# Kernel optimization log

Hardware: AMD Instinct MI355X
Metric: run time of the kernel (lower is better)

## Reference

```python
import jax, jax.numpy as jnp
import numpy as np

N = 100000   # n_nodes (= ninput, identity features)
E = 1600000  # edges per adjacency (avg degree 16)
H = 128      # nhid
EPS = 1e-12


def setup_inputs() -> dict:
    key = jax.random.key(0)
    ks = jax.random.split(key, 24)
    inp = {
        'adj1_rows': jax.random.randint(ks[0], (E,), 0, N),
        'adj1_cols': jax.random.randint(ks[1], (E,), 0, N),
        'adj1_vals': jax.random.uniform(ks[2], (E,), jnp.float32) / 16.0,
        'adj2_rows': jax.random.randint(ks[3], (E,), 0, N),
        'adj2_cols': jax.random.randint(ks[4], (E,), 0, N),
        'adj2_vals': jax.random.uniform(ks[5], (E,), jnp.float32) / 16.0,
    }
    s = 1.0 / np.sqrt(H)
    inp['w1'] = jax.random.uniform(ks[6], (N, H), jnp.float32, -s, s)
    for i in range(2, 10):
        inp[f'w{i}'] = jax.random.uniform(ks[5 + i], (H, H), jnp.float32, -s, s)
    s2 = 1.0 / np.sqrt(2 * H)
    inp['m1'] = jax.random.uniform(ks[15], (H, 2 * H), jnp.float32, -s, s)
    inp['b1'] = jnp.zeros((2 * H,), jnp.float32)
    inp['m2'] = jax.random.uniform(ks[16], (2 * H, 2 * H), jnp.float32, -s2, s2)
    inp['b2'] = jnp.zeros((2 * H,), jnp.float32)
    inp['m3'] = jax.random.uniform(ks[17], (2 * H, 1), jnp.float32, -s2, s2)
    inp['b3'] = jnp.zeros((1,), jnp.float32)
    return inp


def _spmm(rows, cols, vals, x):
    # sparse [N,N] @ dense [N,H] via gather + segment_sum
    return jax.ops.segment_sum(vals[:, None] * x[cols], rows, num_segments=N)


def _l2norm(x):
    # F.normalize(x, p=2, dim=1)
    n = jnp.sqrt(jnp.sum(x * x, axis=1, keepdims=True))
    return x / jnp.maximum(n, EPS)


def _mlp(x, m1, b1, m2, b2, m3, b3):
    # dropout inactive (eval mode) for deterministic reference
    h = jax.nn.relu(x @ m1 + b1)
    h = jax.nn.relu(h @ m2 + b2)
    return h @ m3 + b3  # [N,1]


def _branch(rows, cols, vals, w1, ws, mlp_params):
    x = jax.nn.relu(_spmm(rows, cols, vals, w1))
    x = _l2norm(x)
    score = _mlp(x, *mlp_params)
    for i, w in enumerate(ws):
        x = jax.nn.relu(_spmm(rows, cols, vals, x @ w))
        if i < len(ws) - 1:  # last layer (gc9) is relu only, no normalize
            x = _l2norm(x)
        score = score + _mlp(x, *mlp_params)
    return score


def reference(adj1_rows, adj1_cols, adj1_vals, adj2_rows, adj2_cols, adj2_vals,
              w1, w2, w3, w4, w5, w6, w7, w8, w9,
              m1, b1, m2, b2, m3, b3):
    ws = [w2, w3, w4, w5, w6, w7, w8, w9]
    mlp_params = (m1, b1, m2, b2, m3, b3)
    score1 = _branch(adj1_rows, adj1_cols, adj1_vals, w1, ws, mlp_params)
    score2 = _branch(adj2_rows, adj2_cols, adj2_vals, w1, ws, mlp_params)
    return score1 * score2  # [N,1]
```

## Files before the change

kernel.cpp:

```cpp
#include <hip/hip_runtime.h>
#include <hip/hip_fp16.h>

#define NN 100000
#define NE 1600000
#define HD 128
#define HD2 256

#define NBK 512
#define RPB 196
#define CH  4096
#define CAP 4096

typedef unsigned int u32;
typedef unsigned short u16;
typedef _Float16 half8 __attribute__((ext_vector_type(8)));
typedef float floatx4 __attribute__((ext_vector_type(4)));

static inline int cdiv(int a, int b){ return (a + b - 1) / b; }

__device__ __forceinline__ u32 split_pack(float v){
  __half h;
  if(fabsf(v) < 6.103515625e-05f) h = __ushort_as_half((u16)0);
  else h = __float2half_rn(v);
  float hf = __half2float(h);
  __half l = __float2half_rn((v - hf) * 4096.0f);
  return (u32)__half_as_ushort(h) | ((u32)__half_as_ushort(l) << 16);
}

__global__ void k_setup(const float* __restrict__ w0, const float* __restrict__ w1,
                        const float* __restrict__ w2, const float* __restrict__ w3,
                        const float* __restrict__ w4, const float* __restrict__ w5,
                        const float* __restrict__ w6, const float* __restrict__ w7,
                        const float* __restrict__ m1, const float* __restrict__ m2,
                        u32* __restrict__ wbase, float* __restrict__ sc,
                        int* __restrict__ bcur){
  int bid = blockIdx.x;
  if(bid < 896){
    int idx = bid * 256 + threadIdx.x;
    const float* W; int K, N, local;
    if(idx < 131072){
      int wi = idx >> 14; local = idx & 16383; K = HD; N = HD;
      W = wi == 0 ? w0 : wi == 1 ? w1 : wi == 2 ? w2 : wi == 3 ? w3 :
          wi == 4 ? w4 : wi == 5 ? w5 : wi == 6 ? w6 : w7;
    } else if(idx < 163840){
      local = idx - 131072; K = HD; N = HD2; W = m1;
    } else {
      local = idx - 163840; K = HD2; N = HD2; W = m2;
    }
    int n = local / K, k = local - n * K;
    wbase[idx] = split_pack(W[(size_t)k * N + n]);
  } else if(bid < 896 + 782){
    int i = (bid - 896) * 256 + threadIdx.x;
    if(i < 2 * NN) sc[i] = 0.f;
  } else {
    int i = (bid - 896 - 782) * 256 + threadIdx.x;
    if(i < 2 * NBK) bcur[i] = (i & (NBK - 1)) * CAP;
  }
}

__global__ void k_binscatter(const int* __restrict__ r0a, const int* __restrict__ c0a,
                             const float* __restrict__ v0a,
                             const int* __restrict__ r1a, const int* __restrict__ c1a,
                             const float* __restrict__ v1a,
                             int* __restrict__ bcur,
                             u32* __restrict__ sr0, uint2* __restrict__ sv0,
                             u32* __restrict__ sr1, uint2* __restrict__ sv1){
  __shared__ int cnt[NBK];
  __shared__ int bstart[NBK];
  __shared__ int gbase[NBK];
  __shared__ int sh[256];
  __shared__ u32 srow[CH];
  __shared__ uint2 scvs[CH];
  int z = blockIdx.y;
  const int* rows = z ? r1a : r0a;
  const int* cols = z ? c1a : c0a;
  const float* vals = z ? v1a : v0a;
  int* cur = bcur + z * NBK;
  u32* osr = z ? sr1 : sr0;
  uint2* osv = z ? sv1 : sv0;
  int t = threadIdx.x;
  for(int i = t; i < NBK; i += 256) cnt[i] = 0;
  __syncthreads();
  int e0 = blockIdx.x * CH;
  int total = NE - e0; if(total > CH) total = CH;
  int r_[16], c_[16], b_[16], k_[16]; float v_[16];
  #pragma unroll
  for(int k = 0; k < 16; k++){
    int e = e0 + t + k * 256;
    b_[k] = -1;
    if(e < NE){
      r_[k] = rows[e]; c_[k] = cols[e]; v_[k] = vals[e];
      b_[k] = r_[k] / RPB;
      k_[k] = atomicAdd(&cnt[b_[k]], 1);
    }
  }
  __syncthreads();
  int v0 = cnt[2 * t], v1 = cnt[2 * t + 1];
  int s2 = v0 + v1;
  sh[t] = s2;
  __syncthreads();
  for(int d = 1; d < 256; d <<= 1){
    int tv = (t >= d) ? sh[t - d] : 0;
    __syncthreads();
    sh[t] += tv;
    __syncthreads();
  }
  int excl = sh[t] - s2;
  bstart[2 * t] = excl;
  bstart[2 * t + 1] = excl + v0;
  __syncthreads();
  #pragma unroll
  for(int k = 0; k < 16; k++){
    if(b_[k] >= 0){
      int slot = bstart[b_[k]] + k_[k];
      srow[slot] = (u32)r_[k];
      scvs[slot] = make_uint2((u32)c_[k], __float_as_uint(v_[k]));
    }
  }
  for(int b = t; b < NBK; b += 256){
    int c = cnt[b];
    if(c > 0) gbase[b] = atomicAdd(&cur[b], c);
  }
  __syncthreads();
  for(int i = t; i < total; i += 256){
    u32 r = srow[i];
    int b = (int)r / RPB;
    int dest = gbase[b] + (i - bstart[b]);
    osr[dest] = r;
    osv[dest] = scvs[i];
  }
}

__global__ void k_bucket_scan(const int* __restrict__ bcur, int* __restrict__ bbase,
                              int* __restrict__ c1ptr, int* __restrict__ c2ptr){
  __shared__ int sh[256];
  int z = blockIdx.x;
  const int* cur = bcur + z * NBK;
  int* bb = bbase + z * NBK;
  int t = threadIdx.x;
  int v0 = cur[2 * t]     - (2 * t) * CAP;
  int v1 = cur[2 * t + 1] - (2 * t + 1) * CAP;
  int s2 = v0 + v1;
  sh[t] = s2;
  __syncthreads();
  for(int d = 1; d < 256; d <<= 1){
    int tv = (t >= d) ? sh[t - d] : 0;
    __syncthreads();
    sh[t] += tv;
    __syncthreads();
  }
  int excl = sh[t] - s2;
  bb[2 * t] = excl;
  bb[2 * t + 1] = excl + v0;
  if(t == 0){
    int* rp = z ? c2ptr : c1ptr;
    rp[NN] = NE;
  }
}

__global__ void k_bucket_place(const int* __restrict__ bcur, const int* __restrict__ bbase,
                               const u32* __restrict__ sr0, const uint2* __restrict__ sv0,
                               const u32* __restrict__ sr1, const uint2* __restrict__ sv1,
                               int* __restrict__ c1ptr, int* __restrict__ c2ptr,
                               uint2* __restrict__ e0, uint2* __restrict__ e1){
  __shared__ int hist[RPB];
  __shared__ int cur[RPB];
  __shared__ int rs[RPB + 1];
  __shared__ int sh[256];
  __shared__ u32 srows[CAP];
  __shared__ uint2 est[CAP];
  int z = blockIdx.y;
  int b = blockIdx.x;
  int r0 = b * RPB;
  if(r0 >= NN) return;
  int rend = r0 + RPB; if(rend > NN) rend = NN;
  int nr = rend - r0;
  const u32* sr = z ? sr1 : sr0;
  const uint2* sv = z ? sv1 : sv0;
  int* rp = z ? c2ptr : c1ptr;
  uint2* ecv = z ? e1 : e0;
  int cnt = bcur[z * NBK + b] - b * CAP;
  int base = bbase[z * NBK + b];
  int g = b * CAP;
  int t = threadIdx.x;
  for(int r = t; r < nr; r += 256) hist[r] = 0;
  __syncthreads();
  for(int i = t; i < cnt; i += 256){
    u32 r = sr[g + i];
    srows[i] = r;
    atomicAdd(&hist[(int)r - r0], 1);
  }
  __syncthreads();
  int v = (t < nr) ? hist[t] : 0;
  sh[t] = v;
  __syncthreads();
  for(int d = 1; d < 256; d <<= 1){
    int tv = (t >= d) ? sh[t - d] : 0;
    __syncthreads();
    sh[t] += tv;
    __syncthreads();
  }
  int excl = sh[t] - v;
  if(t < nr){
    rp[r0 + t] = base + excl;
    cur[t] = excl;
    rs[t] = excl;
  }
  if(t == 0) rs[nr] = cnt;
  __syncthreads();
  for(int i = t; i < cnt; i += 256){
    int r = (int)srows[i] - r0;
    int p = atomicAdd(&cur[r], 1);
    est[p] = sv[g + i];
  }
  __syncthreads();
  for(int r = t; r < nr; r += 256){
    int lo = rs[r], hi = lo + hist[r];
    for(int a = lo + 1; a < hi; a++){
      uint2 key = est[a];
      int bb2 = a - 1;
      while(bb2 >= lo && est[bb2].x > key.x){ est[bb2 + 1] = est[bb2]; bb2--; }
      est[bb2 + 1] = key;
    }
  }
  __syncthreads();
  for(int i = t; i < cnt; i += 256) ecv[base + i] = est[i];
}

template<bool NORM>
__global__ void k_spmm(const int* __restrict__ rowptr, const uint2* __restrict__ ecv,
                       const float* __restrict__ X, u32* __restrict__ outpk){
  int node = (blockIdx.x << 2) + (threadIdx.x >> 6);
  int lane = threadIdx.x & 63;
  if(node >= NN) return;
  int h = lane >> 5, s = lane & 31;
  int sb = rowptr[node], e = rowptr[node + 1];
  float ax = 0.f, ay = 0.f, az = 0.f, aw = 0.f;
  int i = sb;
  for(; i + 7 < e; i += 8){
    uint2 ee[4]; float4 xx[4];
    #pragma unroll
    for(int j = 0; j < 4; j++) ee[j] = ecv[i + 2 * j + h];
    #pragma unroll
    for(int j = 0; j < 4; j++) xx[j] = *(const float4*)(X + (size_t)ee[j].x * HD + s * 4);
    #pragma unroll
    for(int j = 0; j < 4; j++){
      float vv = __uint_as_float(ee[j].y);
      ax = fmaf(vv, xx[j].x, ax);
      ay = fmaf(vv, xx[j].y, ay);
      az = fmaf(vv, xx[j].z, az);
      aw = fmaf(vv, xx[j].w, aw);
    }
  }
  for(; i < e; i += 2){
    int idx = i + h;
    bool ok = idx < e;
    uint2 f = ecv[ok ? idx : i];
    float vv = ok ? __uint_as_float(f.y) : 0.f;
    float4 xv = *(const float4*)(X + (size_t)f.x * HD + s * 4);
    ax = fmaf(vv, xv.x, ax);
    ay = fmaf(vv, xv.y, ay);
    az = fmaf(vv, xv.z, az);
    aw = fmaf(vv, xv.w, aw);
  }
  ax += __shfl_xor(ax, 32, 64);
  ay += __shfl_xor(ay, 32, 64);
  az += __shfl_xor(az, 32, 64);
  aw += __shfl_xor(aw, 32, 64);
  ax = fmaxf(ax, 0.f); ay = fmaxf(ay, 0.f);
  az = fmaxf(az, 0.f); aw = fmaxf(aw, 0.f);
  if(NORM){
    float ss = ax * ax + ay * ay + az * az + aw * aw;
    #pragma unroll
    for(int o = 16; o >= 1; o >>= 1) ss += __shfl_xor(ss, o, 64);
    float scale = 1.f / fmaxf(sqrtf(ss), 1e-12f);
    ax *= scale; ay *= scale; az *= scale; aw *= scale;
  }
  if(h == 0){
    uint4 p;
    p.x = split_pack(ax); p.y = split_pack(ay);
    p.z = split_pack(az); p.w = split_pack(aw);
    *(uint4*)(outpk + (size_t)node * HD + s * 4) = p;
  }
}

template<int MODE>
__launch_bounds__(256, 2)
__global__ void k_mfma_gemm(const u32* __restrict__ Apk, const u32* __restrict__ Btpk,
                            const u32* __restrict__ Bt1pk,
                            const float* __restrict__ bias, float* __restrict__ Yout,
                            u32* __restrict__ Hout, const float* __restrict__ m3,
                            float* __restrict__ score, int M, int K, int N){
  __shared__ u16 As_h[128 * 40], As_l[128 * 40];
  __shared__ u16 Bs_h[128 * 40], Bs_l[128 * 40];
  constexpr int NYC = (MODE == 0) ? 1 : ((MODE == 3) ? 3 : 2);
  const int d = blockIdx.x;
  const int grp = d / (8 * NYC);
  const int rem = d - grp * 8 * NYC;
  const int rt = grp * 8 + (rem & 7);
  const int ct = rem >> 3;
  const int nrt = (M + 127) >> 7;
  if(rt >= nrt) return;
  const int tid = threadIdx.x;
  const int lane = tid & 63, wid = tid >> 6;
  const int lm = lane & 15, lg = lane >> 4;
  const int mq = (wid & 1) * 64, nq = (wid >> 1) * 64;
  const int m0 = rt * 128;
  int n0 = ct * 128;
  const u32* Bt = Btpk;
  bool m0path = true;
  if(MODE == 3){
    m0path = (ct == 0);
    if(m0path){ n0 = 0; }
    else      { n0 = (ct - 1) * 128; Bt = Bt1pk; }
  }

  floatx4 accA[4][4], accB[4][4];
  #pragma unroll
  for(int i = 0; i < 4; i++)
    #pragma unroll
    for(int j = 0; j < 4; j++){
      accA[i][j] = (floatx4){0.f, 0.f, 0.f, 0.f};
      accB[i][j] = (floatx4){0.f, 0.f, 0.f, 0.f};
    }

  for(int k0 = 0; k0 < K; k0 += 32){
    uint4 av[4], bv[4];
    #pragma unroll
    for(int j = 0; j < 4; j++){
      int li = tid + j * 256;
      int row = li >> 3, kc = (li & 7) * 4;
      int ar = m0 + row; if(ar >= M) ar = M - 1;
      av[j] = *(const uint4*)(Apk + (size_t)ar * K + k0 + kc);
      bv[j] = *(const uint4*)(Bt + (size_t)(n0 + row) * K + k0 + kc);
    }
    if(k0) __syncthreads();
    #pragma unroll
    for(int j = 0; j < 4; j++){
      int li = tid + j * 256;
      int row = li >> 3, kc = (li & 7) * 4;
      int base = row * 40 + kc;
      ushort4 h, l;
      h.x = (u16)(av[j].x & 0xffff); l.x = (u16)(av[j].x >> 16);
      h.y = (u16)(av[j].y & 0xffff); l.y = (u16)(av[j].y >> 16);
      h.z = (u16)(av[j].z & 0xffff); l.z = (u16)(av[j].z >> 16);
      h.w = (u16)(av[j].w & 0xffff); l.w = (u16)(av[j].w >> 16);
      *(ushort4*)&As_h[base] = h;
      *(ushort4*)&As_l[base] = l;
      h.x = (u16)(bv[j].x & 0xffff); l.x = (u16)(bv[j].x >> 16);
      h.y = (u16)(bv[j].y & 0xffff); l.y = (u16)(bv[j].y >> 16);
      h.z = (u16)(bv[j].z & 0xffff); l.z = (u16)(bv[j].z >> 16);
      h.w = (u16)(bv[j].w & 0xffff); l.w = (u16)(bv[j].w >> 16);
      *(ushort4*)&Bs_h[base] = h;
      *(ushort4*)&Bs_l[base] = l;
    }
    __syncthreads();

    half8 fa_h[4], fa_l[4], fb_h[4], fb_l[4];
    #pragma unroll
    for(int s = 0; s < 4; s++){
      int ra = (mq + s * 16 + lm) * 40 + lg * 8;
      fa_h[s] = *(const half8*)&As_h[ra];
      fa_l[s] = *(const half8*)&As_l[ra];
      int rb = (nq + s * 16 + lm) * 40 + lg * 8;
      fb_h[s] = *(const half8*)&Bs_h[rb];
      fb_l[s] = *(const half8*)&Bs_l[rb];
    }
    #pragma unroll
    for(int i = 0; i < 4; i++)
      #pragma unroll
      for(int j = 0; j < 4; j++){
        accA[i][j] = __builtin_amdgcn_mfma_f32_16x16x32_f16(fa_h[i], fb_h[j], accA[i][j], 0, 0, 0);
        accB[i][j] = __builtin_amdgcn_mfma_f32_16x16x32_f16(fa_h[i], fb_l[j], accB[i][j], 0, 0, 0);
        accB[i][j] = __builtin_amdgcn_mfma_f32_16x16x32_f16(fa_l[i], fb_h[j], accB[i][j], 0, 0, 0);
      }
  }

  const float inv4096 = 1.f / 4096.f;
  if(MODE == 0 || (MODE == 3 && m0path)){
    int ldy = (MODE == 3) ? HD : N;
    #pragma unroll
    for(int i = 0; i < 4; i++)
      #pragma unroll
      for(int r = 0; r < 4; r++){
        int m = m0 + mq + i * 16 + lg * 4 + r;
        if(m < M){
          #pragma unroll
          for(int j = 0; j < 4; j++){
            int c = n0 + nq + j * 16 + lm;
            Yout[(size_t)m * ldy + c] = accA[i][j][r] + accB[i][j][r] * inv4096;
          }
        }
      }
  } else if(MODE == 1 || MODE == 3){
    int ldh = (MODE == 3) ? HD2 : N;
    #pragma unroll
    for(int i = 0; i < 4; i++)
      #pragma unroll
      for(int r = 0; r < 4; r++){
        int m = m0 + mq + i * 16 + lg * 4 + r;
        if(m < M){
          #pragma unroll
          for(int j = 0; j < 4; j++){
            int c = n0 + nq + j * 16 + lm;
            float v = fmaxf(accA[i][j][r] + accB[i][j][r] * inv4096 + bias[c], 0.f);
            Hout[(size_t)m * ldh + c] = split_pack(v);
          }
        }
      }
  } else {
    #pragma unroll
    for(int i = 0; i < 4; i++)
      #pragma unroll
      for(int r = 0; r < 4; r++){
        float s = 0.f;
        #pragma unroll
        for(int j = 0; j < 4; j++){
          int c = n0 + nq + j * 16 + lm;
          float v = fmaxf(accA[i][j][r] + accB[i][j][r] * inv4096 + bias[c], 0.f);
          s = fmaf(v, m3[c], s);
        }
        s += __shfl_xor(s, 1, 64);
        s += __shfl_xor(s, 2, 64);
        s += __shfl_xor(s, 4, 64);
        s += __shfl_xor(s, 8, 64);
        int m = m0 + mq + i * 16 + lg * 4 + r;
        if(lm == 0 && m < M) atomicAdd(&score[m], s);
      }
  }
}

__global__ void k_final(const float* __restrict__ sc, const float* __restrict__ b3,
                        float* __restrict__ out){
  int i = blockIdx.x * 256 + threadIdx.x;
  if(i < NN){
    float b = 9.f * b3[0];
    out[i] = (sc[i] + b) * (sc[NN + i] + b);
  }
}

extern "C" void kernel_launch(void* const* d_in, const int* in_sizes, int n_in,
                              void* d_out, int out_size, void* d_ws, size_t ws_size,
                              hipStream_t stream){
  const int*   a1r = (const int*)d_in[0];
  const int*   a1c = (const int*)d_in[1];
  const float* a1v = (const float*)d_in[2];
  const int*   a2r = (const int*)d_in[3];
  const int*   a2c = (const int*)d_in[4];
  const float* a2v = (const float*)d_in[5];
  const float* w1  = (const float*)d_in[6];
  const float* w[8];
  for(int i = 0; i < 8; i++) w[i] = (const float*)d_in[7 + i];
  const float* m1 = (const float*)d_in[15];
  const float* b1 = (const float*)d_in[16];
  const float* m2 = (const float*)d_in[17];
  const float* b2 = (const float*)d_in[18];
  const float* m3 = (const float*)d_in[19];
  const float* b3 = (const float*)d_in[20];
  float* out = (float*)d_out;

  char* base = (char*)d_ws;
  size_t off = 0;
  auto alloc = [&](size_t bytes) -> char* {
    char* r = base + off;
    off += (bytes + 255) & ~(size_t)255;
    return r;
  };
  int*   c1ptr = (int*)  alloc((size_t)(NN + 1) * 4);
  int*   c2ptr = (int*)  alloc((size_t)(NN + 1) * 4);
  uint2* ecv1  = (uint2*)alloc((size_t)NE * 8);
  uint2* ecv2  = (uint2*)alloc((size_t)NE * 8);
  int*   cursor= (int*)  alloc((size_t)2 * NBK * 4);
  int*   bbase = (int*)  alloc((size_t)2 * NBK * 4);
  float* sc    = (float*)alloc((size_t)2 * NN * 4);
  u32*   wtpk[8];
  for(int i = 0; i < 8; i++) wtpk[i] = (u32*)alloc((size_t)HD * HD * 4);
  u32*   m1tpk = (u32*)alloc((size_t)HD2 * HD * 4);
  u32*   m2tpk = (u32*)alloc((size_t)HD2 * HD2 * 4);
  u32*   xpk   = (u32*)alloc((size_t)NN * HD * 4);
  u32*   h1pk  = (u32*)alloc((size_t)NN * HD2 * 4);
  size_t need_ded = off + (((size_t)NN * HD * 4 + 255) & ~(size_t)255);
  bool ded_y = (ws_size >= need_ded);
  float* y = ded_y ? (float*)alloc((size_t)NN * HD * 4) : (float*)h1pk;

  const size_t SZ = (size_t)NBK * CAP;
  char* hb = (char*)h1pk;
  uint2* sv1 = (uint2*)hb;
  u32*   sr1 = (u32*)(hb + SZ * 8);
  uint2* sv2 = (uint2*)(hb + SZ * 12);
  u32*   sr2 = (u32*)(hb + SZ * 20);

  hipLaunchKernelGGL(k_setup, dim3(896 + 782 + 4), dim3(256), 0, stream,
                     w[0], w[1], w[2], w[3], w[4], w[5], w[6], w[7], m1, m2,
                     wtpk[0], sc, cursor);
  hipLaunchKernelGGL(k_binscatter, dim3(cdiv(NE, CH), 2), dim3(256), 0, stream,
                     a1r, a1c, a1v, a2r, a2c, a2v, cursor, sr1, sv1, sr2, sv2);
  hipLaunchKernelGGL(k_bucket_scan, dim3(2), dim3(256), 0, stream, cursor, bbase, c1ptr, c2ptr);
  hipLaunchKernelGGL(k_bucket_place, dim3(NBK, 2), dim3(256), 0, stream,
                     cursor, bbase, sr1, sv1, sr2, sv2, c1ptr, c2ptr, ecv1, ecv2);

  const int NRT = cdiv(NN, 128);
  const int GP  = cdiv(NRT, 8) * 8;
  const int SPB = cdiv(NN, 4);
  auto mode1 = [&](){
    hipLaunchKernelGGL((k_mfma_gemm<1>), dim3(GP * 2), dim3(256), 0, stream,
                       xpk, m1tpk, (const u32*)nullptr, b1, (float*)nullptr, h1pk,
                       (const float*)nullptr, (float*)nullptr, NN, HD, HD2);
  };
  auto mode2 = [&](float* score){
    hipLaunchKernelGGL((k_mfma_gemm<2>), dim3(GP * 2), dim3(256), 0, stream,
                       h1pk, m2tpk, (const u32*)nullptr, b2, (float*)nullptr, (u32*)nullptr,
                       m3, score, NN, HD2, HD2);
  };
  auto gemm0 = [&](int i){
    hipLaunchKernelGGL((k_mfma_gemm<0>), dim3(GP * 1), dim3(256), 0, stream,
                       xpk, wtpk[i], (const u32*)nullptr, (const float*)nullptr, y, (u32*)nullptr,
                       (const float*)nullptr, (float*)nullptr, NN, HD, HD);
  };
  auto fused01 = [&](int i){
    hipLaunchKernelGGL((k_mfma_gemm<3>), dim3(GP * 3), dim3(256), 0, stream,
                       xpk, wtpk[i], m1tpk, b1, y, h1pk,
                       (const float*)nullptr, (float*)nullptr, NN, HD, 0);
  };

  for(int b = 0; b < 2; b++){
    const int* rp = b ? c2ptr : c1ptr;
    const uint2* ecv = b ? ecv2 : ecv1;
    float* score = sc + (size_t)b * NN;
    hipLaunchKernelGGL((k_spmm<true>), dim3(SPB), dim3(256), 0, stream,
                       rp, ecv, w1, xpk);
    if(ded_y){
      for(int i = 0; i < 8; i++){
        fused01(i);
        mode2(score);
        if(i < 7)
          hipLaunchKernelGGL((k_spmm<true>),  dim3(SPB), dim3(256), 0, stream,
                             rp, ecv, y, xpk);
        else
          hipLaunchKernelGGL((k_spmm<false>), dim3(SPB), dim3(256), 0, stream,
                             rp, ecv, y, xpk);
      }
      mode1();
      mode2(score);
    } else {
      mode1();
      mode2(score);
      for(int i = 0; i < 8; i++){
        gemm0(i);
        if(i < 7)
          hipLaunchKernelGGL((k_spmm<true>),  dim3(SPB), dim3(256), 0, stream,
                             rp, ecv, y, xpk);
        else
          hipLaunchKernelGGL((k_spmm<false>), dim3(SPB), dim3(256), 0, stream,
                             rp, ecv, y, xpk);
        mode1();
        mode2(score);
      }
    }
  }

  hipLaunchKernelGGL(k_final, dim3(cdiv(NN, 256)), dim3(256), 0, stream, sc, b3, out);
}
```

Baseline: 4.268 ms.

## Pre-swizzle weights into MFMA fragment layout and drop per-row edge sort

Weights are now pre-arranged at setup into split high/low half arrays in the exact per-lane MFMA B-fragment order. The GEMM then loads B fragments straight from global memory (L2-resident) instead of staging them through shared memory, which halves LDS usage and removes the B-tile LDS writes. Separately, bucket placement now scatters edges directly to their global CSR slots and skips the per-row insertion sort by column. The edges within a row end up in nondeterministic order, which can change summation order and gather locality.

```diff
diff --git a/kernel.cpp b/kernel.cpp
--- a/kernel.cpp
+++ b/kernel.cpp
@@ -32,23 +32,29 @@
                         const float* __restrict__ w4, const float* __restrict__ w5,
                         const float* __restrict__ w6, const float* __restrict__ w7,
                         const float* __restrict__ m1, const float* __restrict__ m2,
-                        u32* __restrict__ wbase, float* __restrict__ sc,
-                        int* __restrict__ bcur){
+                        u16* __restrict__ bfh, u16* __restrict__ bfl,
+                        float* __restrict__ sc, int* __restrict__ bcur){
   int bid = blockIdx.x;
   if(bid < 896){
     int idx = bid * 256 + threadIdx.x;
-    const float* W; int K, N, local;
+    const float* W; int K, N, e;
     if(idx < 131072){
-      int wi = idx >> 14; local = idx & 16383; K = HD; N = HD;
+      int wi = idx >> 14; e = idx & 16383; K = HD; N = HD;
       W = wi == 0 ? w0 : wi == 1 ? w1 : wi == 2 ? w2 : wi == 3 ? w3 :
           wi == 4 ? w4 : wi == 5 ? w5 : wi == 6 ? w6 : w7;
     } else if(idx < 163840){
-      local = idx - 131072; K = HD; N = HD2; W = m1;
+      e = idx - 131072; K = HD; N = HD2; W = m1;
     } else {
-      local = idx - 163840; K = HD2; N = HD2; W = m2;
-    }
-    int n = local / K, k = local - n * K;
-    wbase[idx] = split_pack(W[(size_t)k * N + n]);
+      e = idx - 163840; K = HD2; N = HD2; W = m2;
+    }
+    int KS = K >> 5;
+    int j = e & 7, lane = (e >> 3) & 63, rest = e >> 9;
+    int ks = rest % KS, nfrag = rest / KS;
+    int c = nfrag * 16 + (lane & 15);
+    int k = ks * 32 + (lane >> 4) * 8 + j;
+    u32 p = split_pack(W[(size_t)k * N + c]);
+    bfh[idx] = (u16)(p & 0xffffu);
+    bfl[idx] = (u16)(p >> 16);
   } else if(bid < 896 + 782){
     int i = (bid - 896) * 256 + threadIdx.x;
     if(i < 2 * NN) sc[i] = 0.f;
@@ -165,10 +171,8 @@
                                uint2* __restrict__ e0, uint2* __restrict__ e1){
   __shared__ int hist[RPB];
   __shared__ int cur[RPB];
-  __shared__ int rs[RPB + 1];
   __shared__ int sh[256];
   __shared__ u32 srows[CAP];
-  __shared__ uint2 est[CAP];
   int z = blockIdx.y;
   int b = blockIdx.x;
   int r0 = b * RPB;
@@ -203,28 +207,14 @@
   int excl = sh[t] - v;
   if(t < nr){
     rp[r0 + t] = base + excl;
-    cur[t] = excl;
-    rs[t] = excl;
-  }
-  if(t == 0) rs[nr] = cnt;
+    cur[t] = base + excl;
+  }
   __syncthreads();
   for(int i = t; i < cnt; i += 256){
     int r = (int)srows[i] - r0;
     int p = atomicAdd(&cur[r], 1);
-    est[p] = sv[g + i];
-  }
-  __syncthreads();
-  for(int r = t; r < nr; r += 256){
-    int lo = rs[r], hi = lo + hist[r];
-    for(int a = lo + 1; a < hi; a++){
-      uint2 key = est[a];
-      int bb2 = a - 1;
-      while(bb2 >= lo && est[bb2].x > key.x){ est[bb2 + 1] = est[bb2]; bb2--; }
-      est[bb2 + 1] = key;
-    }
-  }
-  __syncthreads();
-  for(int i = t; i < cnt; i += 256) ecv[base + i] = est[i];
+    ecv[p] = sv[g + i];
+  }
 }
 
 template<bool NORM>
@@ -286,13 +276,13 @@
 
 template<int MODE>
 __launch_bounds__(256, 2)
-__global__ void k_mfma_gemm(const u32* __restrict__ Apk, const u32* __restrict__ Btpk,
-                            const u32* __restrict__ Bt1pk,
+__global__ void k_mfma_gemm(const u32* __restrict__ Apk,
+                            const u16* __restrict__ BGh, const u16* __restrict__ BGl,
+                            const u16* __restrict__ B1Gh, const u16* __restrict__ B1Gl,
                             const float* __restrict__ bias, float* __restrict__ Yout,
                             u32* __restrict__ Hout, const float* __restrict__ m3,
                             float* __restrict__ score, int M, int K, int N){
   __shared__ u16 As_h[128 * 40], As_l[128 * 40];
-  __shared__ u16 Bs_h[128 * 40], Bs_l[128 * 40];
   constexpr int NYC = (MODE == 0) ? 1 : ((MODE == 3) ? 3 : 2);
   const int d = blockIdx.x;
   const int grp = d / (8 * NYC);
@@ -307,13 +297,15 @@
   const int mq = (wid & 1) * 64, nq = (wid >> 1) * 64;
   const int m0 = rt * 128;
   int n0 = ct * 128;
-  const u32* Bt = Btpk;
+  const u16* Bh = BGh; const u16* Bl = BGl;
   bool m0path = true;
   if(MODE == 3){
     m0path = (ct == 0);
     if(m0path){ n0 = 0; }
-    else      { n0 = (ct - 1) * 128; Bt = Bt1pk; }
-  }
+    else      { n0 = (ct - 1) * 128; Bh = B1Gh; Bl = B1Gl; }
+  }
+  const int KS = K >> 5;
+  const int nf0 = (n0 + nq) >> 4;
 
   floatx4 accA[4][4], accB[4][4];
   #pragma unroll
@@ -324,15 +316,14 @@
       accB[i][j] = (floatx4){0.f, 0.f, 0.f, 0.f};
     }
 
-  for(int k0 = 0; k0 < K; k0 += 32){
-    uint4 av[4], bv[4];
+  for(int k0 = 0, ks = 0; k0 < K; k0 += 32, ks++){
+    uint4 av[4];
     #pragma unroll
     for(int j = 0; j < 4; j++){
       int li = tid + j * 256;
       int row = li >> 3, kc = (li & 7) * 4;
       int ar = m0 + row; if(ar >= M) ar = M - 1;
       av[j] = *(const uint4*)(Apk + (size_t)ar * K + k0 + kc);
-      bv[j] = *(const uint4*)(Bt + (size_t)(n0 + row) * K + k0 + kc);
     }
     if(k0) __syncthreads();
     #pragma unroll
@@ -347,24 +338,23 @@
       h.w = (u16)(av[j].w & 0xffff); l.w = (u16)(av[j].w >> 16);
       *(ushort4*)&As_h[base] = h;
       *(ushort4*)&As_l[base] = l;
-      h.x = (u16)(bv[j].x & 0xffff); l.x = (u16)(bv[j].x >> 16);
-      h.y = (u16)(bv[j].y & 0xffff); l.y = (u16)(bv[j].y >> 16);
-      h.z = (u16)(bv[j].z & 0xffff); l.z = (u16)(bv[j].z >> 16);
-      h.w = (u16)(bv[j].w & 0xffff); l.w = (u16)(bv[j].w >> 16);
-      *(ushort4*)&Bs_h[base] = h;
-      *(ushort4*)&Bs_l[base] = l;
     }
     __syncthreads();
 
     half8 fa_h[4], fa_l[4], fb_h[4], fb_l[4];
+    {
+      size_t bo = (((size_t)nf0 * KS + ks) << 9) + lane * 8;
+      #pragma unroll
+      for(int s = 0; s < 4; s++){
+        fb_h[s] = *(const half8*)(Bh + bo + (((size_t)s * KS) << 9));
+        fb_l[s] = *(const half8*)(Bl + bo + (((size_t)s * KS) << 9));
+      }
+    }
     #pragma unroll
     for(int s = 0; s < 4; s++){
       int ra = (mq + s * 16 + lm) * 40 + lg * 8;
       fa_h[s] = *(const half8*)&As_h[ra];
       fa_l[s] = *(const half8*)&As_l[ra];
-      int rb = (nq + s * 16 + lm) * 40 + lg * 8;
-      fb_h[s] = *(const half8*)&Bs_h[rb];
-      fb_l[s] = *(const half8*)&Bs_l[rb];
     }
     #pragma unroll
     for(int i = 0; i < 4; i++)
@@ -473,15 +463,16 @@
   int*   cursor= (int*)  alloc((size_t)2 * NBK * 4);
   int*   bbase = (int*)  alloc((size_t)2 * NBK * 4);
   float* sc    = (float*)alloc((size_t)2 * NN * 4);
-  u32*   wtpk[8];
-  for(int i = 0; i < 8; i++) wtpk[i] = (u32*)alloc((size_t)HD * HD * 4);
-  u32*   m1tpk = (u32*)alloc((size_t)HD2 * HD * 4);
-  u32*   m2tpk = (u32*)alloc((size_t)HD2 * HD2 * 4);
+  u16*   bfh   = (u16*)  alloc((size_t)229376 * 2);
+  u16*   bfl   = (u16*)  alloc((size_t)229376 * 2);
   u32*   xpk   = (u32*)alloc((size_t)NN * HD * 4);
   u32*   h1pk  = (u32*)alloc((size_t)NN * HD2 * 4);
   size_t need_ded = off + (((size_t)NN * HD * 4 + 255) & ~(size_t)255);
   bool ded_y = (ws_size >= need_ded);
   float* y = ded_y ? (float*)alloc((size_t)NN * HD * 4) : (float*)h1pk;
+
+  const u16* m1h = bfh + 131072; const u16* m1l = bfl + 131072;
+  const u16* m2h = bfh + 163840; const u16* m2l = bfl + 163840;
 
   const size_t SZ = (size_t)NBK * CAP;
   char* hb = (char*)h1pk;
@@ -492,7 +483,7 @@
 
   hipLaunchKernelGGL(k_setup, dim3(896 + 782 + 4), dim3(256), 0, stream,
                      w[0], w[1], w[2], w[3], w[4], w[5], w[6], w[7], m1, m2,
-                     wtpk[0], sc, cursor);
+                     bfh, bfl, sc, cursor);
   hipLaunchKernelGGL(k_binscatter, dim3(cdiv(NE, CH), 2), dim3(256), 0, stream,
                      a1r, a1c, a1v, a2r, a2c, a2v, cursor, sr1, sv1, sr2, sv2);
   hipLaunchKernelGGL(k_bucket_scan, dim3(2), dim3(256), 0, stream, cursor, bbase, c1ptr, c2ptr);
@@ -504,22 +495,27 @@
   const int SPB = cdiv(NN, 4);
   auto mode1 = [&](){
     hipLaunchKernelGGL((k_mfma_gemm<1>), dim3(GP * 2), dim3(256), 0, stream,
-                       xpk, m1tpk, (const u32*)nullptr, b1, (float*)nullptr, h1pk,
+                       xpk, m1h, m1l, (const u16*)nullptr, (const u16*)nullptr,
+                       b1, (float*)nullptr, h1pk,
                        (const float*)nullptr, (float*)nullptr, NN, HD, HD2);
   };
   auto mode2 = [&](float* score){
     hipLaunchKernelGGL((k_mfma_gemm<2>), dim3(GP * 2), dim3(256), 0, stream,
-                       h1pk, m2tpk, (const u32*)nullptr, b2, (float*)nullptr, (u32*)nullptr,
+                       h1pk, m2h, m2l, (const u16*)nullptr, (const u16*)nullptr,
+                       b2, (float*)nullptr, (u32*)nullptr,
                        m3, score, NN, HD2, HD2);
   };
   auto gemm0 = [&](int i){
     hipLaunchKernelGGL((k_mfma_gemm<0>), dim3(GP * 1), dim3(256), 0, stream,
-                       xpk, wtpk[i], (const u32*)nullptr, (const float*)nullptr, y, (u32*)nullptr,
+                       xpk, bfh + (size_t)i * 16384, bfl + (size_t)i * 16384,
+                       (const u16*)nullptr, (const u16*)nullptr,
+                       (const float*)nullptr, y, (u32*)nullptr,
                        (const float*)nullptr, (float*)nullptr, NN, HD, HD);
   };
   auto fused01 = [&](int i){
     hipLaunchKernelGGL((k_mfma_gemm<3>), dim3(GP * 3), dim3(256), 0, stream,
-                       xpk, wtpk[i], m1tpk, b1, y, h1pk,
+                       xpk, bfh + (size_t)i * 16384, bfl + (size_t)i * 16384,
+                       m1h, m1l, b1, y, h1pk,
                        (const float*)nullptr, (float*)nullptr, NN, HD, 0);
   };
 
```

After: 4.358 ms. +2.1%, slower.
